# Optimization experiments

Measured on AMD Instinct MI355X. Metric: run time of the kernel, lower is better.

The kernel has to match this reference:

```python
import jax, jax.numpy as jnp
from jax import lax
import numpy as np

EPS = 1e-3  # Keras BatchNormalization default epsilon

def cond_conv(x, experts, rw, rb):
    # x: [B,H,W,Cin]; experts: [E,kh,kw,Cin,Cout]
    pooled = jnp.mean(x, axis=(1, 2))                       # [B,Cin]
    route = jax.nn.sigmoid(pooled @ rw + rb)                # [B,E]
    kernels = jnp.einsum('be,ehwio->bhwio', route, experts) # per-example kernel
    def conv1(xi, ki):
        return lax.conv_general_dilated(
            xi[None], ki, window_strides=(1, 1), padding='SAME',
            dimension_numbers=('NHWC', 'HWIO', 'NHWC'))[0]
    return jax.vmap(conv1)(x, kernels)

def bn_inf(x, gamma, beta, mean, var):
    inv = gamma * lax.rsqrt(var + EPS)
    return x * inv + (beta - mean * inv)

def maxpool2(x):
    return lax.reduce_window(x, -jnp.inf, lax.max,
                             (1, 2, 2, 1), (1, 2, 2, 1), 'SAME')

def se_block(x, w1, w2):
    s = jnp.mean(x, axis=(1, 2))          # [B,C]
    s = jax.nn.relu(s @ w1)
    s = jax.nn.sigmoid(s @ w2)
    return x * s[:, None, None, :]

def setup_inputs() -> dict:
    key = jax.random.key(0)
    ks = jax.random.split(key, 12)
    d = {
        'x': jax.random.normal(ks[0], (64, 128, 128, 6), jnp.float32),
        'experts1': jax.random.normal(ks[1], (3, 3, 3, 6, 32), jnp.float32) * 0.1,
        'route1_w': jax.random.normal(ks[2], (6, 3), jnp.float32) * 0.1,
        'route1_b': jnp.zeros((3,), jnp.float32),
        'bn1_gamma': jnp.ones((32,), jnp.float32), 'bn1_beta': jnp.zeros((32,), jnp.float32),
        'bn1_mean': jnp.zeros((32,), jnp.float32), 'bn1_var': jnp.ones((32,), jnp.float32),
        'se1_w1': jax.random.normal(ks[3], (32, 2), jnp.float32) * 0.1,
        'se1_w2': jax.random.normal(ks[4], (2, 32), jnp.float32) * 0.1,
        'experts2': jax.random.normal(ks[5], (3, 3, 3, 32, 64), jnp.float32) * 0.05,
        'route2_w': jax.random.normal(ks[6], (32, 3), jnp.float32) * 0.1,
        'route2_b': jnp.zeros((3,), jnp.float32),
        'bn2_gamma': jnp.ones((64,), jnp.float32), 'bn2_beta': jnp.zeros((64,), jnp.float32),
        'bn2_mean': jnp.zeros((64,), jnp.float32), 'bn2_var': jnp.ones((64,), jnp.float32),
        'se2_w1': jax.random.normal(ks[7], (64, 4), jnp.float32) * 0.1,
        'se2_w2': jax.random.normal(ks[8], (4, 64), jnp.float32) * 0.1,
        'experts3': jax.random.normal(ks[9], (3, 3, 3, 64, 128), jnp.float32) * 0.05,
        'route3_w': jax.random.normal(ks[10], (64, 3), jnp.float32) * 0.1,
        'route3_b': jnp.zeros((3,), jnp.float32),
        'bn3_gamma': jnp.ones((128,), jnp.float32), 'bn3_beta': jnp.zeros((128,), jnp.float32),
        'bn3_mean': jnp.zeros((128,), jnp.float32), 'bn3_var': jnp.ones((128,), jnp.float32),
    }
    return d

def reference(x, experts1, route1_w, route1_b, bn1_gamma, bn1_beta, bn1_mean, bn1_var,
              se1_w1, se1_w2, experts2, route2_w, route2_b, bn2_gamma, bn2_beta,
              bn2_mean, bn2_var, se2_w1, se2_w2, experts3, route3_w, route3_b,
              bn3_gamma, bn3_beta, bn3_mean, bn3_var):
    h = cond_conv(x, experts1, route1_w, route1_b)
    h = jax.nn.relu(bn_inf(h, bn1_gamma, bn1_beta, bn1_mean, bn1_var))
    h = maxpool2(h)                       # [B,64,64,32]
    h = se_block(h, se1_w1, se1_w2)
    h = cond_conv(h, experts2, route2_w, route2_b)
    h = jax.nn.relu(bn_inf(h, bn2_gamma, bn2_beta, bn2_mean, bn2_var))
    h = maxpool2(h)                       # [B,32,32,64]
    h = se_block(h, se2_w1, se2_w2)
    h = cond_conv(h, experts3, route3_w, route3_b)
    h = bn_inf(h, bn3_gamma, bn3_beta, bn3_mean, bn3_var)
    return jnp.mean(h, axis=(1, 2))       # [B,128]
```

## Files before the change

### kernel.cpp

```cpp
#include <hip/hip_runtime.h>

#define EPSBN 1e-3f

typedef unsigned short ushort_t;
typedef __attribute__((ext_vector_type(8))) short bf8;
typedef __attribute__((ext_vector_type(4))) float f4;

__device__ __forceinline__ float sigmoidf_(float z) {
  return 1.0f / (1.0f + expf(-z));
}

__device__ __forceinline__ ushort_t f2bf(float x) {
  union { float f; unsigned u; } v; v.f = x;
  unsigned r = (v.u + 0x7fffu + ((v.u >> 16) & 1u)) >> 16;
  return (ushort_t)r;
}

__global__ void k_mean_x(const float* __restrict__ x, float* __restrict__ part) {
  const int b = blockIdx.x >> 2;
  const int q = blockIdx.x & 3;
  const int tid = threadIdx.x;
  float acc[6] = {0.f, 0.f, 0.f, 0.f, 0.f, 0.f};
  const float* xb = x + (size_t)b * 98304 + (size_t)q * 24576;
  for (int p = 0; p < 4; ++p) {
    const float* base = xb + (size_t)p * 6144 + (size_t)tid * 24;
#pragma unroll
    for (int k = 0; k < 6; ++k) {
      const float4 v = *(const float4*)(base + k * 4);
      acc[(4 * k + 0) % 6] += v.x;
      acc[(4 * k + 1) % 6] += v.y;
      acc[(4 * k + 2) % 6] += v.z;
      acc[(4 * k + 3) % 6] += v.w;
    }
  }
#pragma unroll
  for (int c = 0; c < 6; ++c)
    for (int off = 32; off > 0; off >>= 1) acc[c] += __shfl_down(acc[c], off, 64);
  __shared__ float red[4][6];
  const int lane = tid & 63, w = tid >> 6;
  if (lane == 0) {
#pragma unroll
    for (int c = 0; c < 6; ++c) red[w][c] = acc[c];
  }
  __syncthreads();
  if (tid < 6) {
    part[blockIdx.x * 6 + tid] = red[0][tid] + red[1][tid] + red[2][tid] + red[3][tid];
  }
}

__global__ __launch_bounds__(256)
void k_conv1(const float* __restrict__ x, const float* __restrict__ meanx_part,
             const float* __restrict__ experts1,
             const float* __restrict__ rw, const float* __restrict__ rbias,
             const float* __restrict__ gamma, const float* __restrict__ beta,
             const float* __restrict__ bnmean, const float* __restrict__ bnvar,
             ushort_t* __restrict__ p1b, float* __restrict__ part_m1) {
  const int bid = blockIdx.x;
  const int b = bid >> 3;
  const int tyi = (bid >> 1) & 3;
  const int txi = bid & 1;
  __shared__ __align__(16) ushort_t patch[34 * 68 * 8];
  __shared__ float route_s[3];
  __shared__ float mred[4][32];
  const int tid = threadIdx.x;
  const float* xb = x + (size_t)b * (128 * 128 * 6);

  if (tid < 3) {
    float z = rbias[tid];
    for (int c = 0; c < 6; ++c) {
      const float s = meanx_part[(b * 4 + 0) * 6 + c] + meanx_part[(b * 4 + 1) * 6 + c] +
                      meanx_part[(b * 4 + 2) * 6 + c] + meanx_part[(b * 4 + 3) * 6 + c];
      z += (s * (1.0f / 16384.0f)) * rw[c * 3 + tid];
    }
    route_s[tid] = sigmoidf_(z);
  }

  for (int v = tid; v < 34 * 68; v += 256) {
    const int ry = v / 68, p = v - ry * 68;
    const int gy = tyi * 32 - 1 + ry, gx = txi * 64 - 1 + p;
    uint4 u = make_uint4(0u, 0u, 0u, 0u);
    if (((unsigned)gy < 128u) && ((unsigned)gx < 128u)) {
      const float* s = xb + ((size_t)(gy * 128 + gx)) * 6;
      const float2 a0 = *(const float2*)s;
      const float2 a1 = *(const float2*)(s + 2);
      const float2 a2 = *(const float2*)(s + 4);
      u.x = (unsigned)f2bf(a0.x) | ((unsigned)f2bf(a0.y) << 16);
      u.y = (unsigned)f2bf(a1.x) | ((unsigned)f2bf(a1.y) << 16);
      u.z = (unsigned)f2bf(a2.x) | ((unsigned)f2bf(a2.y) << 16);
      u.w = 0u;
    }
    *(uint4*)(patch + (size_t)v * 8) = u;
  }
  __syncthreads();

  const int w = tid >> 6;
  const int lane = tid & 63;
  const int lx = lane & 15, lg = lane >> 4;

  const float r0 = route_s[0], r1 = route_s[1], r2 = route_s[2];
  const int co0 = lx, co1 = 16 + lx;
  const float inv0 = gamma[co0] * rsqrtf(bnvar[co0] + EPSBN);
  const float bias0 = beta[co0] - bnmean[co0] * inv0;
  const float inv1 = gamma[co1] * rsqrtf(bnvar[co1] + EPSBN);
  const float bias1 = beta[co1] - bnmean[co1] * inv1;

  bf8 Bf[3][2];
#pragma unroll
  for (int ky = 0; ky < 3; ++ky) {
#pragma unroll
    for (int nt = 0; nt < 2; ++nt) {
      const int co = nt * 16 + lx;
      const float inv = nt ? inv1 : inv0;
#pragma unroll
      for (int j = 0; j < 8; ++j) {
        float val = 0.f;
        if (j < 6 && lg < 3) {
          const int idx = ((ky * 3 + lg) * 6 + j) * 32 + co;
          val = (r0 * experts1[idx] + r1 * experts1[1728 + idx] +
                 r2 * experts1[3456 + idx]) * inv;
        }
        Bf[ky][nt][j] = (short)f2bf(val);
      }
    }
  }

  float msum0 = 0.f, msum1 = 0.f;

#pragma unroll
  for (int xt = 0; xt < 4; ++xt) {
    bf8 Af[10];
#pragma unroll
    for (int r = 0; r < 10; ++r)
      Af[r] = *(const bf8*)(patch + ((size_t)(w * 8 + r) * 68 + xt * 16 + lx + lg) * 8);
#pragma unroll
    for (int rp = 0; rp < 4; ++rp) {
      const int prow = tyi * 16 + w * 4 + rp;
      f4 acc0[2], acc1[2];
#pragma unroll
      for (int nt = 0; nt < 2; ++nt) {
        acc0[nt] = (f4){0.f, 0.f, 0.f, 0.f};
        acc1[nt] = (f4){0.f, 0.f, 0.f, 0.f};
      }
#pragma unroll
      for (int ky = 0; ky < 3; ++ky) {
#pragma unroll
        for (int nt = 0; nt < 2; ++nt) {
          acc0[nt] = __builtin_amdgcn_mfma_f32_16x16x32_bf16(Af[rp * 2 + ky], Bf[ky][nt], acc0[nt], 0, 0, 0);
          acc1[nt] = __builtin_amdgcn_mfma_f32_16x16x32_bf16(Af[rp * 2 + ky + 1], Bf[ky][nt], acc1[nt], 0, 0, 0);
        }
      }
#pragma unroll
      for (int nt = 0; nt < 2; ++nt) {
        const float bias = nt ? bias1 : bias0;
        const int co = nt * 16 + lx;
#pragma unroll
        for (int q = 0; q < 2; ++q) {
          const float m0 = fmaxf(acc0[nt][2 * q] + bias, 0.f);
          const float m1 = fmaxf(acc0[nt][2 * q + 1] + bias, 0.f);
          const float m2 = fmaxf(acc1[nt][2 * q] + bias, 0.f);
          const float m3 = fmaxf(acc1[nt][2 * q + 1] + bias, 0.f);
          const float mx = fmaxf(fmaxf(m0, m1), fmaxf(m2, m3));
          if (nt) msum1 += mx; else msum0 += mx;
          const int pcol = txi * 32 + xt * 8 + lg * 2 + q;
          p1b[(((size_t)b * 64 + prow) * 64 + pcol) * 32 + co] = f2bf(mx);
        }
      }
    }
  }

  msum0 += __shfl_xor(msum0, 16, 64);
  msum0 += __shfl_xor(msum0, 32, 64);
  msum1 += __shfl_xor(msum1, 16, 64);
  msum1 += __shfl_xor(msum1, 32, 64);
  if (lg == 0) {
    mred[w][lx] = msum0;
    mred[w][16 + lx] = msum1;
  }
  __syncthreads();
  if (tid < 32) {
    part_m1[(size_t)bid * 32 + tid] =
        mred[0][tid] + mred[1][tid] + mred[2][tid] + mred[3][tid];
  }
}

__global__ void k_buildk2(const float* __restrict__ part_m1,
                          const float* __restrict__ experts2,
                          const float* __restrict__ rw, const float* __restrict__ rb,
                          const float* __restrict__ w1, const float* __restrict__ w2,
                          const float* __restrict__ gamma, const float* __restrict__ var,
                          ushort_t* __restrict__ k2pb) {
  const int b = blockIdx.x / 3;
  const int seg = blockIdx.x - b * 3;
  const int tid = threadIdx.x;
  __shared__ float m1[32], h[2], s1[32], route[3];
  if (tid < 32) {
    float s = 0.f;
#pragma unroll
    for (int k = 0; k < 8; ++k) s += part_m1[(size_t)(b * 8 + k) * 32 + tid];
    m1[tid] = s * (1.0f / 4096.0f);
  }
  __syncthreads();
  if (tid < 2) {
    float z = 0.f;
    for (int c = 0; c < 32; ++c) z += m1[c] * w1[c * 2 + tid];
    h[tid] = fmaxf(z, 0.f);
  }
  __syncthreads();
  if (tid < 32) s1[tid] = sigmoidf_(h[0] * w2[tid] + h[1] * w2[32 + tid]);
  __syncthreads();
  if (tid < 3) {
    float z = rb[tid];
    for (int c = 0; c < 32; ++c) z += m1[c] * s1[c] * rw[c * 3 + tid];
    route[tid] = sigmoidf_(z);
  }
  __syncthreads();
  const float r0 = route[0], r1 = route[1], r2 = route[2];
  const int t_lo = seg * 6144, t_hi = t_lo + 6144;
  for (int t = t_lo + tid; t < t_hi; t += 256) {
    const int co = t & 63;
    const int ci = (t >> 6) & 31;
    const int tap = t >> 11;
    const float inv = gamma[co] * rsqrtf(var[co] + EPSBN);
    const float v = r0 * experts2[t] + r1 * experts2[18432 + t] + r2 * experts2[2 * 18432 + t];
    k2pb[(size_t)b * 18432 + ((size_t)tap * 64 + co) * 32 + ci] = f2bf(v * s1[ci] * inv);
  }
}

__global__ __launch_bounds__(256)
void k_conv2(const ushort_t* __restrict__ p1b, const ushort_t* __restrict__ k2pb,
             const float* __restrict__ gamma, const float* __restrict__ beta,
             const float* __restrict__ bnmean, const float* __restrict__ bnvar,
             float* __restrict__ part_s3) {
  const int bi = blockIdx.x;
  const int b = bi >> 5;
  const int tile = (bi >> 1) & 15;
  const int cog = bi & 1;
  const int ty = tile >> 2, tx = tile & 3;
  __shared__ __align__(16) short smem[24480];
  short* As = smem;
  short* Bs = smem + 12960;
  const int tid = threadIdx.x;

  const ushort_t* pb = p1b + (size_t)b * 131072;
  for (int v = tid; v < 1296; v += 256) {
    const int cell = v >> 2, part = v & 3;
    const int ly = cell / 18, lx2 = cell - ly * 18;
    const int gy = ty * 16 - 1 + ly, gx = tx * 16 - 1 + lx2;
    uint4 d = make_uint4(0u, 0u, 0u, 0u);
    if (((unsigned)gy < 64u) && ((unsigned)gx < 64u))
      d = *(const uint4*)(pb + (((size_t)gy << 6) + gx) * 32 + part * 8);
    *(uint4*)(As + (ly * 18 + lx2) * 40 + part * 8) = d;
  }
  for (int v = tid; v < 1152; v += 256) {
    const int r = v >> 2, part = v & 3;
    const int t = r >> 5, n = r & 31;
    const uint4 d = *(const uint4*)(k2pb + (size_t)b * 18432 +
                                    ((size_t)(t * 64 + cog * 32 + n)) * 32 + part * 8);
    *(uint4*)(Bs + r * 40 + part * 8) = d;
  }
  __syncthreads();

  const int w = tid >> 6;
  const int lane = tid & 63;
  const int lx = lane & 15, lg = lane >> 4;

  f4 acc[4][2];
#pragma unroll
  for (int mt = 0; mt < 4; ++mt)
#pragma unroll
    for (int nt = 0; nt < 2; ++nt)
      acc[mt][nt] = (f4){0.f, 0.f, 0.f, 0.f};

#pragma unroll
  for (int kx = 0; kx < 3; ++kx) {
    bf8 Af[6];
#pragma unroll
    for (int r = 0; r < 6; ++r)
      Af[r] = *(const bf8*)(As + ((4 * w + r) * 18 + lx + kx) * 40 + (lg << 3));
#pragma unroll
    for (int ky = 0; ky < 3; ++ky) {
      const int t = ky * 3 + kx;
      const bf8 Bf0 = *(const bf8*)(Bs + ((t << 5) + lx) * 40 + (lg << 3));
      const bf8 Bf1 = *(const bf8*)(Bs + ((t << 5) + 16 + lx) * 40 + (lg << 3));
#pragma unroll
      for (int mt = 0; mt < 4; ++mt) {
        acc[mt][0] = __builtin_amdgcn_mfma_f32_16x16x32_bf16(Af[ky + mt], Bf0, acc[mt][0], 0, 0, 0);
        acc[mt][1] = __builtin_amdgcn_mfma_f32_16x16x32_bf16(Af[ky + mt], Bf1, acc[mt][1], 0, 0, 0);
      }
    }
  }

  float inv[2], bias[2];
#pragma unroll
  for (int nt = 0; nt < 2; ++nt) {
    const int co = cog * 32 + nt * 16 + lx;
    inv[nt] = gamma[co] * rsqrtf(bnvar[co] + EPSBN);
    bias[nt] = beta[co] - bnmean[co] * inv[nt];
  }
  float agg[2][9];
#pragma unroll
  for (int nt = 0; nt < 2; ++nt)
#pragma unroll
    for (int a = 0; a < 9; ++a) agg[nt][a] = 0.f;

#pragma unroll
  for (int half = 0; half < 2; ++half) {
    const int prow = ty * 8 + 2 * w + half;
    const bool rT = (prow == 0), rB = (prow == 31);
#pragma unroll
    for (int q = 0; q < 2; ++q) {
      const int pcol = tx * 8 + 2 * lg + q;
      const bool cL = (pcol == 0), cR = (pcol == 31);
#pragma unroll
      for (int nt = 0; nt < 2; ++nt) {
        const float m0 = fmaxf(acc[2 * half][nt][2 * q] + bias[nt], 0.f);
        const float m1 = fmaxf(acc[2 * half][nt][2 * q + 1] + bias[nt], 0.f);
        const float m2 = fmaxf(acc[2 * half + 1][nt][2 * q] + bias[nt], 0.f);
        const float m3 = fmaxf(acc[2 * half + 1][nt][2 * q + 1] + bias[nt], 0.f);
        const float mx = fmaxf(fmaxf(m0, m1), fmaxf(m2, m3));
        agg[nt][0] += mx;
        if (rT) agg[nt][1] += mx;
        if (rB) agg[nt][2] += mx;
        if (cL) agg[nt][3] += mx;
        if (cR) agg[nt][4] += mx;
        if (rT && cL) agg[nt][5] += mx;
        if (rT && cR) agg[nt][6] += mx;
        if (rB && cL) agg[nt][7] += mx;
        if (rB && cR) agg[nt][8] += mx;
      }
    }
  }

#pragma unroll
  for (int nt = 0; nt < 2; ++nt)
#pragma unroll
    for (int a = 0; a < 9; ++a) {
      float v = agg[nt][a];
      v += __shfl_xor(v, 16, 64);
      v += __shfl_xor(v, 32, 64);
      agg[nt][a] = v;
    }
  __syncthreads();
  float* sred = (float*)smem;
  if (lg == 0) {
#pragma unroll
    for (int nt = 0; nt < 2; ++nt)
#pragma unroll
      for (int a = 0; a < 9; ++a)
        sred[((w * 2 + nt) * 16 + lx) * 9 + a] = agg[nt][a];
  }
  __syncthreads();
  for (int v = tid; v < 288; v += 256) {
    const int a = v >> 5;
    const int colocal = v & 31;
    const int nt = colocal >> 4, lxx = colocal & 15;
    float s = 0.f;
#pragma unroll
    for (int ww = 0; ww < 4; ++ww) s += sred[((ww * 2 + nt) * 16 + lxx) * 9 + a];
    part_s3[(size_t)bi * 288 + v] = s;
  }
}

__global__ __launch_bounds__(512)
void k_final(const float* __restrict__ part_s3, const float* __restrict__ experts3,
             const float* __restrict__ rw, const float* __restrict__ rb,
             const float* __restrict__ w1, const float* __restrict__ w2,
             const float* __restrict__ gamma, const float* __restrict__ beta,
             const float* __restrict__ bnmean, const float* __restrict__ bnvar,
             float* __restrict__ out) {
  const int b = blockIdx.x;
  const int tid = threadIdx.x;
  __shared__ float AG[9][64], Sp[9][64], m2[64], h[4], s2[64], route[3], redf[4][128];

  for (int v = tid; v < 576; v += 512) {
    const int a = v >> 6, ci = v & 63;
    const int cg = ci >> 5, colocal = ci & 31;
    float s = 0.f;
#pragma unroll
    for (int tile = 0; tile < 16; ++tile)
      s += part_s3[(size_t)((b * 16 + tile) * 2 + cg) * 288 + a * 32 + colocal];
    AG[a][ci] = s;
  }
  __syncthreads();
  if (tid < 64) m2[tid] = AG[0][tid] * (1.0f / 1024.0f);
  __syncthreads();
  if (tid < 4) {
    float z = 0.f;
    for (int c = 0; c < 64; ++c) z += m2[c] * w1[c * 4 + tid];
    h[tid] = fmaxf(z, 0.f);
  }
  __syncthreads();
  if (tid < 64) {
    float z = 0.f;
#pragma unroll
    for (int j = 0; j < 4; ++j) z += h[j] * w2[j * 64 + tid];
    s2[tid] = sigmoidf_(z);
  }
  __syncthreads();
  if (tid < 3) {
    float z = rb[tid];
    for (int c = 0; c < 64; ++c) z += m2[c] * s2[c] * rw[c * 3 + tid];
    route[tid] = sigmoidf_(z);
  }
  __syncthreads();
  for (int v = tid; v < 576; v += 512) {
    const int tap = v >> 6, ci = v & 63;
    const int ky = tap / 3, kx = tap - 3 * ky;
    const float T = AG[0][ci];
    const float A = (ky == 0) ? AG[2][ci] : ((ky == 2) ? AG[1][ci] : 0.f);
    const float B = (kx == 0) ? AG[4][ci] : ((kx == 2) ? AG[3][ci] : 0.f);
    float AB = 0.f;
    if (ky == 0 && kx == 0) AB = AG[8][ci];
    else if (ky == 0 && kx == 2) AB = AG[7][ci];
    else if (ky == 2 && kx == 0) AB = AG[6][ci];
    else if (ky == 2 && kx == 2) AB = AG[5][ci];
    Sp[tap][ci] = (T - A - B + AB) * s2[ci];
  }
  __syncthreads();

  const int co = tid & 127;
  const int quarter = tid >> 7;
  const int tap_lo = (quarter == 0) ? 0 : (2 * quarter + 1);
  const int tap_hi = tap_lo + ((quarter == 0) ? 3 : 2);
  float acc = 0.f;
#pragma unroll
  for (int e = 0; e < 3; ++e) {
    float m = 0.f;
    for (int tap = tap_lo; tap < tap_hi; ++tap) {
      const float* E = experts3 + ((size_t)(e * 9 + tap) * 64) * 128 + co;
#pragma unroll 16
      for (int ci = 0; ci < 64; ++ci) m = fmaf(E[(size_t)ci * 128], Sp[tap][ci], m);
    }
    acc += route[e] * m;
  }
  redf[quarter][co] = acc;
  __syncthreads();
  if (tid < 128) {
    const float total = redf[0][tid] + redf[1][tid] + redf[2][tid] + redf[3][tid];
    const float inv = gamma[tid] * rsqrtf(bnvar[tid] + EPSBN);
    out[(size_t)b * 128 + tid] = total * (1.0f / 1024.0f) * inv + (beta[tid] - bnmean[tid] * inv);
  }
}

extern "C" void kernel_launch(void* const* d_in, const int* in_sizes, int n_in,
                              void* d_out, int out_size, void* d_ws, size_t ws_size,
                              hipStream_t stream) {
  const float* x        = (const float*)d_in[0];
  const float* experts1 = (const float*)d_in[1];
  const float* rw1      = (const float*)d_in[2];
  const float* rb1      = (const float*)d_in[3];
  const float* g1  = (const float*)d_in[4];
  const float* be1 = (const float*)d_in[5];
  const float* mu1 = (const float*)d_in[6];
  const float* va1 = (const float*)d_in[7];
  const float* sw1a = (const float*)d_in[8];
  const float* sw1b = (const float*)d_in[9];
  const float* experts2 = (const float*)d_in[10];
  const float* rw2 = (const float*)d_in[11];
  const float* rb2 = (const float*)d_in[12];
  const float* g2  = (const float*)d_in[13];
  const float* be2 = (const float*)d_in[14];
  const float* mu2 = (const float*)d_in[15];
  const float* va2 = (const float*)d_in[16];
  const float* sw2a = (const float*)d_in[17];
  const float* sw2b = (const float*)d_in[18];
  const float* experts3 = (const float*)d_in[19];
  const float* rw3 = (const float*)d_in[20];
  const float* rb3 = (const float*)d_in[21];
  const float* g3  = (const float*)d_in[22];
  const float* be3 = (const float*)d_in[23];
  const float* mu3 = (const float*)d_in[24];
  const float* va3 = (const float*)d_in[25];
  float* out = (float*)d_out;
  float* ws = (float*)d_ws;

  float* meanx_part = ws;
  float* part_m1    = ws + 1536;
  ushort_t* k2pb    = (ushort_t*)(ws + 17920);
  float* part_s3    = ws + 607744;
  ushort_t* p1b     = (ushort_t*)(ws + 1197568);

  hipLaunchKernelGGL(k_mean_x, dim3(256), dim3(256), 0, stream, x, meanx_part);
  hipLaunchKernelGGL(k_conv1, dim3(512), dim3(256), 0, stream,
                     x, meanx_part, experts1, rw1, rb1, g1, be1, mu1, va1, p1b, part_m1);
  hipLaunchKernelGGL(k_buildk2, dim3(192), dim3(256), 0, stream,
                     part_m1, experts2, rw2, rb2, sw1a, sw1b, g2, va2, k2pb);
  hipLaunchKernelGGL(k_conv2, dim3(2048), dim3(256), 0, stream,
                     p1b, k2pb, g2, be2, mu2, va2, part_s3);
  hipLaunchKernelGGL(k_final, dim3(64), dim3(512), 0, stream,
                     part_s3, experts3, rw3, rb3, sw2a, sw2b, g3, be3, mu3, va3, out);
}
```

Before: 187.9 us.

## Fuse all stages into one cooperative kernel with per-batch spin barriers

```diff
diff --git a/kernel.cpp b/kernel.cpp
--- a/kernel.cpp
+++ b/kernel.cpp
@@ -16,429 +16,442 @@
   return (ushort_t)r;
 }
 
-__global__ void k_mean_x(const float* __restrict__ x, float* __restrict__ part) {
-  const int b = blockIdx.x >> 2;
-  const int q = blockIdx.x & 3;
+__device__ __forceinline__ void batch_barrier(unsigned* ctr, unsigned target) {
+  __syncthreads();
+  if (threadIdx.x == 0) {
+    __threadfence();
+    atomicAdd(ctr, 1u);
+    while (atomicAdd(ctr, 0u) < target) __builtin_amdgcn_s_sleep(2);
+    __threadfence();
+  }
+  __syncthreads();
+}
+
+__global__ __launch_bounds__(256, 2)
+void k_fused(const float* __restrict__ x,
+             const float* __restrict__ experts1,
+             const float* __restrict__ rw1, const float* __restrict__ rb1,
+             const float* __restrict__ g1, const float* __restrict__ be1,
+             const float* __restrict__ mu1, const float* __restrict__ va1,
+             const float* __restrict__ sw1a, const float* __restrict__ sw1b,
+             const float* __restrict__ experts2,
+             const float* __restrict__ rw2, const float* __restrict__ rb2,
+             const float* __restrict__ g2, const float* __restrict__ be2,
+             const float* __restrict__ mu2, const float* __restrict__ va2,
+             const float* __restrict__ sw2a, const float* __restrict__ sw2b,
+             const float* __restrict__ experts3,
+             const float* __restrict__ rw3, const float* __restrict__ rb3,
+             const float* __restrict__ g3, const float* __restrict__ be3,
+             const float* __restrict__ mu3, const float* __restrict__ va3,
+             float* __restrict__ out,
+             float* __restrict__ meanx_part, float* __restrict__ part_m1,
+             ushort_t* __restrict__ k2pb, float* __restrict__ part_s3,
+             ushort_t* __restrict__ p1b, unsigned* __restrict__ bctr) {
+  __shared__ __align__(16) unsigned char smem[53568];
+  const int bid = blockIdx.x;
+  const int b = bid >> 3;
+  const int sub = bid & 7;
   const int tid = threadIdx.x;
-  float acc[6] = {0.f, 0.f, 0.f, 0.f, 0.f, 0.f};
-  const float* xb = x + (size_t)b * 98304 + (size_t)q * 24576;
-  for (int p = 0; p < 4; ++p) {
-    const float* base = xb + (size_t)p * 6144 + (size_t)tid * 24;
-#pragma unroll
-    for (int k = 0; k < 6; ++k) {
+  unsigned* ctr = bctr + b;
+
+  {
+    float acc[6] = {0.f, 0.f, 0.f, 0.f, 0.f, 0.f};
+    const float* base = x + (size_t)b * 98304 + (size_t)sub * 12288 + (size_t)tid * 48;
+#pragma unroll
+    for (int k = 0; k < 12; ++k) {
       const float4 v = *(const float4*)(base + k * 4);
       acc[(4 * k + 0) % 6] += v.x;
       acc[(4 * k + 1) % 6] += v.y;
       acc[(4 * k + 2) % 6] += v.z;
       acc[(4 * k + 3) % 6] += v.w;
     }
+#pragma unroll
+    for (int c = 0; c < 6; ++c)
+      for (int off = 32; off > 0; off >>= 1) acc[c] += __shfl_down(acc[c], off, 64);
+    float* red0 = (float*)smem;
+    const int lane = tid & 63, w = tid >> 6;
+    if (lane == 0) {
+#pragma unroll
+      for (int c = 0; c < 6; ++c) red0[w * 6 + c] = acc[c];
+    }
+    __syncthreads();
+    if (tid < 6)
+      meanx_part[bid * 6 + tid] = red0[tid] + red0[6 + tid] + red0[12 + tid] + red0[18 + tid];
   }
-#pragma unroll
-  for (int c = 0; c < 6; ++c)
-    for (int off = 32; off > 0; off >>= 1) acc[c] += __shfl_down(acc[c], off, 64);
-  __shared__ float red[4][6];
-  const int lane = tid & 63, w = tid >> 6;
-  if (lane == 0) {
-#pragma unroll
-    for (int c = 0; c < 6; ++c) red[w][c] = acc[c];
+  batch_barrier(ctr, 8u);
+
+  {
+    ushort_t* patch = (ushort_t*)smem;
+    float* route_s = (float*)(smem + 36992);
+    float* mred = (float*)(smem + 37008);
+    const int tyi = sub >> 1, txi = sub & 1;
+    const float* xb = x + (size_t)b * 98304;
+
+    if (tid < 3) {
+      float z = rb1[tid];
+      for (int c = 0; c < 6; ++c) {
+        float s = 0.f;
+#pragma unroll
+        for (int k = 0; k < 8; ++k) s += meanx_part[(b * 8 + k) * 6 + c];
+        z += (s * (1.0f / 16384.0f)) * rw1[c * 3 + tid];
+      }
+      route_s[tid] = sigmoidf_(z);
+    }
+
+    for (int v = tid; v < 34 * 68; v += 256) {
+      const int ry = v / 68, p = v - ry * 68;
+      const int gy = tyi * 32 - 1 + ry, gx = txi * 64 - 1 + p;
+      uint4 u = make_uint4(0u, 0u, 0u, 0u);
+      if (((unsigned)gy < 128u) && ((unsigned)gx < 128u)) {
+        const float* s = xb + ((size_t)(gy * 128 + gx)) * 6;
+        const float2 a0 = *(const float2*)s;
+        const float2 a1 = *(const float2*)(s + 2);
+        const float2 a2 = *(const float2*)(s + 4);
+        u.x = (unsigned)f2bf(a0.x) | ((unsigned)f2bf(a0.y) << 16);
+        u.y = (unsigned)f2bf(a1.x) | ((unsigned)f2bf(a1.y) << 16);
+        u.z = (unsigned)f2bf(a2.x) | ((unsigned)f2bf(a2.y) << 16);
+        u.w = 0u;
+      }
+      *(uint4*)(patch + (size_t)v * 8) = u;
+    }
+    __syncthreads();
+
+    const int w = tid >> 6;
+    const int lane = tid & 63;
+    const int lx = lane & 15, lg = lane >> 4;
+
+    const float r0 = route_s[0], r1 = route_s[1], r2 = route_s[2];
+    const int co0 = lx, co1 = 16 + lx;
+    const float inv0 = g1[co0] * rsqrtf(va1[co0] + EPSBN);
+    const float bias0 = be1[co0] - mu1[co0] * inv0;
+    const float inv1 = g1[co1] * rsqrtf(va1[co1] + EPSBN);
+    const float bias1 = be1[co1] - mu1[co1] * inv1;
+
+    bf8 Bf[3][2];
+#pragma unroll
+    for (int ky = 0; ky < 3; ++ky) {
+#pragma unroll
+      for (int nt = 0; nt < 2; ++nt) {
+        const int co = nt * 16 + lx;
+        const float inv = nt ? inv1 : inv0;
+#pragma unroll
+        for (int j = 0; j < 8; ++j) {
+          float val = 0.f;
+          if (j < 6 && lg < 3) {
+            const int idx = ((ky * 3 + lg) * 6 + j) * 32 + co;
+            val = (r0 * experts1[idx] + r1 * experts1[1728 + idx] +
+                   r2 * experts1[3456 + idx]) * inv;
+          }
+          Bf[ky][nt][j] = (short)f2bf(val);
+        }
+      }
+    }
+
+    float msum0 = 0.f, msum1 = 0.f;
+#pragma unroll
+    for (int xt = 0; xt < 4; ++xt) {
+      bf8 Af[10];
+#pragma unroll
+      for (int r = 0; r < 10; ++r)
+        Af[r] = *(const bf8*)(patch + ((size_t)(w * 8 + r) * 68 + xt * 16 + lx + lg) * 8);
+#pragma unroll
+      for (int rp = 0; rp < 4; ++rp) {
+        const int prow = tyi * 16 + w * 4 + rp;
+        f4 acc0[2], acc1[2];
+#pragma unroll
+        for (int nt = 0; nt < 2; ++nt) {
+          acc0[nt] = (f4){0.f, 0.f, 0.f, 0.f};
+          acc1[nt] = (f4){0.f, 0.f, 0.f, 0.f};
+        }
+#pragma unroll
+        for (int ky = 0; ky < 3; ++ky) {
+#pragma unroll
+          for (int nt = 0; nt < 2; ++nt) {
+            acc0[nt] = __builtin_amdgcn_mfma_f32_16x16x32_bf16(Af[rp * 2 + ky], Bf[ky][nt], acc0[nt], 0, 0, 0);
+            acc1[nt] = __builtin_amdgcn_mfma_f32_16x16x32_bf16(Af[rp * 2 + ky + 1], Bf[ky][nt], acc1[nt], 0, 0, 0);
+          }
+        }
+#pragma unroll
+        for (int nt = 0; nt < 2; ++nt) {
+          const float bias = nt ? bias1 : bias0;
+          const int co = nt * 16 + lx;
+#pragma unroll
+          for (int q = 0; q < 2; ++q) {
+            const float m0 = fmaxf(acc0[nt][2 * q] + bias, 0.f);
+            const float m1 = fmaxf(acc0[nt][2 * q + 1] + bias, 0.f);
+            const float m2 = fmaxf(acc1[nt][2 * q] + bias, 0.f);
+            const float m3 = fmaxf(acc1[nt][2 * q + 1] + bias, 0.f);
+            const float mx = fmaxf(fmaxf(m0, m1), fmaxf(m2, m3));
+            if (nt) msum1 += mx; else msum0 += mx;
+            const int pcol = txi * 32 + xt * 8 + lg * 2 + q;
+            p1b[(((size_t)b * 64 + prow) * 64 + pcol) * 32 + co] = f2bf(mx);
+          }
+        }
+      }
+    }
+
+    msum0 += __shfl_xor(msum0, 16, 64);
+    msum0 += __shfl_xor(msum0, 32, 64);
+    msum1 += __shfl_xor(msum1, 16, 64);
+    msum1 += __shfl_xor(msum1, 32, 64);
+    if (lg == 0) {
+      mred[w * 32 + lx] = msum0;
+      mred[w * 32 + 16 + lx] = msum1;
+    }
+    __syncthreads();
+    if (tid < 32) {
+      part_m1[(size_t)bid * 32 + tid] =
+          mred[tid] + mred[32 + tid] + mred[64 + tid] + mred[96 + tid];
+    }
   }
-  __syncthreads();
-  if (tid < 6) {
-    part[blockIdx.x * 6 + tid] = red[0][tid] + red[1][tid] + red[2][tid] + red[3][tid];
+  batch_barrier(ctr, 16u);
+
+  {
+    float* m1 = (float*)smem;
+    float* h = m1 + 32;
+    float* s1 = h + 4;
+    float* route = s1 + 32;
+    if (tid < 32) {
+      float s = 0.f;
+#pragma unroll
+      for (int k = 0; k < 8; ++k) s += part_m1[(size_t)(b * 8 + k) * 32 + tid];
+      m1[tid] = s * (1.0f / 4096.0f);
+    }
+    __syncthreads();
+    if (tid < 2) {
+      float z = 0.f;
+      for (int c = 0; c < 32; ++c) z += m1[c] * sw1a[c * 2 + tid];
+      h[tid] = fmaxf(z, 0.f);
+    }
+    __syncthreads();
+    if (tid < 32) s1[tid] = sigmoidf_(h[0] * sw1b[tid] + h[1] * sw1b[32 + tid]);
+    __syncthreads();
+    if (tid < 3) {
+      float z = rb2[tid];
+      for (int c = 0; c < 32; ++c) z += m1[c] * s1[c] * rw2[c * 3 + tid];
+      route[tid] = sigmoidf_(z);
+    }
+    __syncthreads();
+    const float r0 = route[0], r1 = route[1], r2 = route[2];
+    const int t_lo = sub * 2304, t_hi = t_lo + 2304;
+    for (int t = t_lo + tid; t < t_hi; t += 256) {
+      const int co = t & 63;
+      const int ci = (t >> 6) & 31;
+      const int tap = t >> 11;
+      const float inv = g2[co] * rsqrtf(va2[co] + EPSBN);
+      const float v = r0 * experts2[t] + r1 * experts2[18432 + t] + r2 * experts2[2 * 18432 + t];
+      k2pb[(size_t)b * 18432 + ((size_t)tap * 64 + co) * 32 + ci] = f2bf(v * s1[ci] * inv);
+    }
   }
-}
-
-__global__ __launch_bounds__(256)
-void k_conv1(const float* __restrict__ x, const float* __restrict__ meanx_part,
-             const float* __restrict__ experts1,
-             const float* __restrict__ rw, const float* __restrict__ rbias,
-             const float* __restrict__ gamma, const float* __restrict__ beta,
-             const float* __restrict__ bnmean, const float* __restrict__ bnvar,
-             ushort_t* __restrict__ p1b, float* __restrict__ part_m1) {
-  const int bid = blockIdx.x;
-  const int b = bid >> 3;
-  const int tyi = (bid >> 1) & 3;
-  const int txi = bid & 1;
-  __shared__ __align__(16) ushort_t patch[34 * 68 * 8];
-  __shared__ float route_s[3];
-  __shared__ float mred[4][32];
-  const int tid = threadIdx.x;
-  const float* xb = x + (size_t)b * (128 * 128 * 6);
-
-  if (tid < 3) {
-    float z = rbias[tid];
-    for (int c = 0; c < 6; ++c) {
-      const float s = meanx_part[(b * 4 + 0) * 6 + c] + meanx_part[(b * 4 + 1) * 6 + c] +
-                      meanx_part[(b * 4 + 2) * 6 + c] + meanx_part[(b * 4 + 3) * 6 + c];
-      z += (s * (1.0f / 16384.0f)) * rw[c * 3 + tid];
-    }
-    route_s[tid] = sigmoidf_(z);
+  batch_barrier(ctr, 24u);
+
+  {
+    short* As = (short*)smem;
+    short* Bs = As + 12960;
+    float* sred = (float*)(smem + 48960);
+    const int w = tid >> 6;
+    const int lane = tid & 63;
+    const int lx = lane & 15, lg = lane >> 4;
+    const ushort_t* pb = p1b + (size_t)b * 131072;
+
+    for (int cc = 0; cc < 4; ++cc) {
+      const int ti = sub * 4 + cc;
+      const int tile = ti >> 1, cog = ti & 1;
+      const int ty = tile >> 2, tx2 = tile & 3;
+      __syncthreads();
+      for (int v = tid; v < 1296; v += 256) {
+        const int cell = v >> 2, part = v & 3;
+        const int ly = cell / 18, lx2 = cell - ly * 18;
+        const int gy = ty * 16 - 1 + ly, gx = tx2 * 16 - 1 + lx2;
+        uint4 d = make_uint4(0u, 0u, 0u, 0u);
+        if (((unsigned)gy < 64u) && ((unsigned)gx < 64u))
+          d = *(const uint4*)(pb + (((size_t)gy << 6) + gx) * 32 + part * 8);
+        *(uint4*)(As + (ly * 18 + lx2) * 40 + part * 8) = d;
+      }
+      for (int v = tid; v < 1152; v += 256) {
+        const int r = v >> 2, part = v & 3;
+        const int t = r >> 5, n = r & 31;
+        const uint4 d = *(const uint4*)(k2pb + (size_t)b * 18432 +
+                                        ((size_t)(t * 64 + cog * 32 + n)) * 32 + part * 8);
+        *(uint4*)(Bs + r * 40 + part * 8) = d;
+      }
+      __syncthreads();
+
+      f4 acc[4][2];
+#pragma unroll
+      for (int mt = 0; mt < 4; ++mt)
+#pragma unroll
+        for (int nt = 0; nt < 2; ++nt)
+          acc[mt][nt] = (f4){0.f, 0.f, 0.f, 0.f};
+
+#pragma unroll
+      for (int kx = 0; kx < 3; ++kx) {
+        bf8 Af[6];
+#pragma unroll
+        for (int r = 0; r < 6; ++r)
+          Af[r] = *(const bf8*)(As + ((4 * w + r) * 18 + lx + kx) * 40 + (lg << 3));
+#pragma unroll
+        for (int ky = 0; ky < 3; ++ky) {
+          const int t = ky * 3 + kx;
+          const bf8 Bf0 = *(const bf8*)(Bs + ((t << 5) + lx) * 40 + (lg << 3));
+          const bf8 Bf1 = *(const bf8*)(Bs + ((t << 5) + 16 + lx) * 40 + (lg << 3));
+#pragma unroll
+          for (int mt = 0; mt < 4; ++mt) {
+            acc[mt][0] = __builtin_amdgcn_mfma_f32_16x16x32_bf16(Af[ky + mt], Bf0, acc[mt][0], 0, 0, 0);
+            acc[mt][1] = __builtin_amdgcn_mfma_f32_16x16x32_bf16(Af[ky + mt], Bf1, acc[mt][1], 0, 0, 0);
+          }
+        }
+      }
+
+      float inv[2], bias[2];
+#pragma unroll
+      for (int nt = 0; nt < 2; ++nt) {
+        const int co = cog * 32 + nt * 16 + lx;
+        inv[nt] = g2[co] * rsqrtf(va2[co] + EPSBN);
+        bias[nt] = be2[co] - mu2[co] * inv[nt];
+      }
+      float agg[2][9];
+#pragma unroll
+      for (int nt = 0; nt < 2; ++nt)
+#pragma unroll
+        for (int a = 0; a < 9; ++a) agg[nt][a] = 0.f;
+
+#pragma unroll
+      for (int half = 0; half < 2; ++half) {
+        const int prow = ty * 8 + 2 * w + half;
+        const bool rT = (prow == 0), rB = (prow == 31);
+#pragma unroll
+        for (int q = 0; q < 2; ++q) {
+          const int pcol = tx2 * 8 + 2 * lg + q;
+          const bool cL = (pcol == 0), cR = (pcol == 31);
+#pragma unroll
+          for (int nt = 0; nt < 2; ++nt) {
+            const float m0 = fmaxf(acc[2 * half][nt][2 * q] + bias[nt], 0.f);
+            const float m1 = fmaxf(acc[2 * half][nt][2 * q + 1] + bias[nt], 0.f);
+            const float m2 = fmaxf(acc[2 * half + 1][nt][2 * q] + bias[nt], 0.f);
+            const float m3 = fmaxf(acc[2 * half + 1][nt][2 * q + 1] + bias[nt], 0.f);
+            const float mx = fmaxf(fmaxf(m0, m1), fmaxf(m2, m3));
+            agg[nt][0] += mx;
+            if (rT) agg[nt][1] += mx;
+            if (rB) agg[nt][2] += mx;
+            if (cL) agg[nt][3] += mx;
+            if (cR) agg[nt][4] += mx;
+            if (rT && cL) agg[nt][5] += mx;
+            if (rT && cR) agg[nt][6] += mx;
+            if (rB && cL) agg[nt][7] += mx;
+            if (rB && cR) agg[nt][8] += mx;
+          }
+        }
+      }
+
+#pragma unroll
+      for (int nt = 0; nt < 2; ++nt)
+#pragma unroll
+        for (int a = 0; a < 9; ++a) {
+          float v = agg[nt][a];
+          v += __shfl_xor(v, 16, 64);
+          v += __shfl_xor(v, 32, 64);
+          agg[nt][a] = v;
+        }
+      if (lg == 0) {
+#pragma unroll
+        for (int nt = 0; nt < 2; ++nt)
+#pragma unroll
+          for (int a = 0; a < 9; ++a)
+            sred[((w * 2 + nt) * 16 + lx) * 9 + a] = agg[nt][a];
+      }
+      __syncthreads();
+      for (int v = tid; v < 288; v += 256) {
+        const int a = v >> 5;
+        const int colocal = v & 31;
+        const int nt = colocal >> 4, lxx = colocal & 15;
+        float s = 0.f;
+#pragma unroll
+        for (int ww = 0; ww < 4; ++ww) s += sred[((ww * 2 + nt) * 16 + lxx) * 9 + a];
+        part_s3[(size_t)(b * 32 + ti) * 288 + v] = s;
+      }
+    }
   }
-
-  for (int v = tid; v < 34 * 68; v += 256) {
-    const int ry = v / 68, p = v - ry * 68;
-    const int gy = tyi * 32 - 1 + ry, gx = txi * 64 - 1 + p;
-    uint4 u = make_uint4(0u, 0u, 0u, 0u);
-    if (((unsigned)gy < 128u) && ((unsigned)gx < 128u)) {
-      const float* s = xb + ((size_t)(gy * 128 + gx)) * 6;
-      const float2 a0 = *(const float2*)s;
-      const float2 a1 = *(const float2*)(s + 2);
-      const float2 a2 = *(const float2*)(s + 4);
-      u.x = (unsigned)f2bf(a0.x) | ((unsigned)f2bf(a0.y) << 16);
-      u.y = (unsigned)f2bf(a1.x) | ((unsigned)f2bf(a1.y) << 16);
-      u.z = (unsigned)f2bf(a2.x) | ((unsigned)f2bf(a2.y) << 16);
-      u.w = 0u;
-    }
-    *(uint4*)(patch + (size_t)v * 8) = u;
-  }
-  __syncthreads();
-
-  const int w = tid >> 6;
-  const int lane = tid & 63;
-  const int lx = lane & 15, lg = lane >> 4;
-
-  const float r0 = route_s[0], r1 = route_s[1], r2 = route_s[2];
-  const int co0 = lx, co1 = 16 + lx;
-  const float inv0 = gamma[co0] * rsqrtf(bnvar[co0] + EPSBN);
-  const float bias0 = beta[co0] - bnmean[co0] * inv0;
-  const float inv1 = gamma[co1] * rsqrtf(bnvar[co1] + EPSBN);
-  const float bias1 = beta[co1] - bnmean[co1] * inv1;
-
-  bf8 Bf[3][2];
-#pragma unroll
-  for (int ky = 0; ky < 3; ++ky) {
-#pragma unroll
-    for (int nt = 0; nt < 2; ++nt) {
-      const int co = nt * 16 + lx;
-      const float inv = nt ? inv1 : inv0;
-#pragma unroll
-      for (int j = 0; j < 8; ++j) {
-        float val = 0.f;
-        if (j < 6 && lg < 3) {
-          const int idx = ((ky * 3 + lg) * 6 + j) * 32 + co;
-          val = (r0 * experts1[idx] + r1 * experts1[1728 + idx] +
-                 r2 * experts1[3456 + idx]) * inv;
-        }
-        Bf[ky][nt][j] = (short)f2bf(val);
-      }
-    }
-  }
-
-  float msum0 = 0.f, msum1 = 0.f;
-
-#pragma unroll
-  for (int xt = 0; xt < 4; ++xt) {
-    bf8 Af[10];
-#pragma unroll
-    for (int r = 0; r < 10; ++r)
-      Af[r] = *(const bf8*)(patch + ((size_t)(w * 8 + r) * 68 + xt * 16 + lx + lg) * 8);
-#pragma unroll
-    for (int rp = 0; rp < 4; ++rp) {
-      const int prow = tyi * 16 + w * 4 + rp;
-      f4 acc0[2], acc1[2];
-#pragma unroll
-      for (int nt = 0; nt < 2; ++nt) {
-        acc0[nt] = (f4){0.f, 0.f, 0.f, 0.f};
-        acc1[nt] = (f4){0.f, 0.f, 0.f, 0.f};
-      }
-#pragma unroll
-      for (int ky = 0; ky < 3; ++ky) {
-#pragma unroll
-        for (int nt = 0; nt < 2; ++nt) {
-          acc0[nt] = __builtin_amdgcn_mfma_f32_16x16x32_bf16(Af[rp * 2 + ky], Bf[ky][nt], acc0[nt], 0, 0, 0);
-          acc1[nt] = __builtin_amdgcn_mfma_f32_16x16x32_bf16(Af[rp * 2 + ky + 1], Bf[ky][nt], acc1[nt], 0, 0, 0);
-        }
-      }
-#pragma unroll
-      for (int nt = 0; nt < 2; ++nt) {
-        const float bias = nt ? bias1 : bias0;
-        const int co = nt * 16 + lx;
-#pragma unroll
-        for (int q = 0; q < 2; ++q) {
-          const float m0 = fmaxf(acc0[nt][2 * q] + bias, 0.f);
-          const float m1 = fmaxf(acc0[nt][2 * q + 1] + bias, 0.f);
-          const float m2 = fmaxf(acc1[nt][2 * q] + bias, 0.f);
-          const float m3 = fmaxf(acc1[nt][2 * q + 1] + bias, 0.f);
-          const float mx = fmaxf(fmaxf(m0, m1), fmaxf(m2, m3));
-          if (nt) msum1 += mx; else msum0 += mx;
-          const int pcol = txi * 32 + xt * 8 + lg * 2 + q;
-          p1b[(((size_t)b * 64 + prow) * 64 + pcol) * 32 + co] = f2bf(mx);
-        }
-      }
-    }
-  }
-
-  msum0 += __shfl_xor(msum0, 16, 64);
-  msum0 += __shfl_xor(msum0, 32, 64);
-  msum1 += __shfl_xor(msum1, 16, 64);
-  msum1 += __shfl_xor(msum1, 32, 64);
-  if (lg == 0) {
-    mred[w][lx] = msum0;
-    mred[w][16 + lx] = msum1;
-  }
-  __syncthreads();
-  if (tid < 32) {
-    part_m1[(size_t)bid * 32 + tid] =
-        mred[0][tid] + mred[1][tid] + mred[2][tid] + mred[3][tid];
-  }
-}
-
-__global__ void k_buildk2(const float* __restrict__ part_m1,
-                          const float* __restrict__ experts2,
-                          const float* __restrict__ rw, const float* __restrict__ rb,
-                          const float* __restrict__ w1, const float* __restrict__ w2,
-                          const float* __restrict__ gamma, const float* __restrict__ var,
-                          ushort_t* __restrict__ k2pb) {
-  const int b = blockIdx.x / 3;
-  const int seg = blockIdx.x - b * 3;
-  const int tid = threadIdx.x;
-  __shared__ float m1[32], h[2], s1[32], route[3];
-  if (tid < 32) {
-    float s = 0.f;
-#pragma unroll
-    for (int k = 0; k < 8; ++k) s += part_m1[(size_t)(b * 8 + k) * 32 + tid];
-    m1[tid] = s * (1.0f / 4096.0f);
-  }
-  __syncthreads();
-  if (tid < 2) {
-    float z = 0.f;
-    for (int c = 0; c < 32; ++c) z += m1[c] * w1[c * 2 + tid];
-    h[tid] = fmaxf(z, 0.f);
-  }
-  __syncthreads();
-  if (tid < 32) s1[tid] = sigmoidf_(h[0] * w2[tid] + h[1] * w2[32 + tid]);
-  __syncthreads();
-  if (tid < 3) {
-    float z = rb[tid];
-    for (int c = 0; c < 32; ++c) z += m1[c] * s1[c] * rw[c * 3 + tid];
-    route[tid] = sigmoidf_(z);
-  }
-  __syncthreads();
-  const float r0 = route[0], r1 = route[1], r2 = route[2];
-  const int t_lo = seg * 6144, t_hi = t_lo + 6144;
-  for (int t = t_lo + tid; t < t_hi; t += 256) {
-    const int co = t & 63;
-    const int ci = (t >> 6) & 31;
-    const int tap = t >> 11;
-    const float inv = gamma[co] * rsqrtf(var[co] + EPSBN);
-    const float v = r0 * experts2[t] + r1 * experts2[18432 + t] + r2 * experts2[2 * 18432 + t];
-    k2pb[(size_t)b * 18432 + ((size_t)tap * 64 + co) * 32 + ci] = f2bf(v * s1[ci] * inv);
-  }
-}
-
-__global__ __launch_bounds__(256)
-void k_conv2(const ushort_t* __restrict__ p1b, const ushort_t* __restrict__ k2pb,
-             const float* __restrict__ gamma, const float* __restrict__ beta,
-             const float* __restrict__ bnmean, const float* __restrict__ bnvar,
-             float* __restrict__ part_s3) {
-  const int bi = blockIdx.x;
-  const int b = bi >> 5;
-  const int tile = (bi >> 1) & 15;
-  const int cog = bi & 1;
-  const int ty = tile >> 2, tx = tile & 3;
-  __shared__ __align__(16) short smem[24480];
-  short* As = smem;
-  short* Bs = smem + 12960;
-  const int tid = threadIdx.x;
-
-  const ushort_t* pb = p1b + (size_t)b * 131072;
-  for (int v = tid; v < 1296; v += 256) {
-    const int cell = v >> 2, part = v & 3;
-    const int ly = cell / 18, lx2 = cell - ly * 18;
-    const int gy = ty * 16 - 1 + ly, gx = tx * 16 - 1 + lx2;
-    uint4 d = make_uint4(0u, 0u, 0u, 0u);
-    if (((unsigned)gy < 64u) && ((unsigned)gx < 64u))
-      d = *(const uint4*)(pb + (((size_t)gy << 6) + gx) * 32 + part * 8);
-    *(uint4*)(As + (ly * 18 + lx2) * 40 + part * 8) = d;
-  }
-  for (int v = tid; v < 1152; v += 256) {
-    const int r = v >> 2, part = v & 3;
-    const int t = r >> 5, n = r & 31;
-    const uint4 d = *(const uint4*)(k2pb + (size_t)b * 18432 +
-                                    ((size_t)(t * 64 + cog * 32 + n)) * 32 + part * 8);
-    *(uint4*)(Bs + r * 40 + part * 8) = d;
-  }
-  __syncthreads();
-
-  const int w = tid >> 6;
-  const int lane = tid & 63;
-  const int lx = lane & 15, lg = lane >> 4;
-
-  f4 acc[4][2];
-#pragma unroll
-  for (int mt = 0; mt < 4; ++mt)
-#pragma unroll
-    for (int nt = 0; nt < 2; ++nt)
-      acc[mt][nt] = (f4){0.f, 0.f, 0.f, 0.f};
-
-#pragma unroll
-  for (int kx = 0; kx < 3; ++kx) {
-    bf8 Af[6];
-#pragma unroll
-    for (int r = 0; r < 6; ++r)
-      Af[r] = *(const bf8*)(As + ((4 * w + r) * 18 + lx + kx) * 40 + (lg << 3));
-#pragma unroll
-    for (int ky = 0; ky < 3; ++ky) {
-      const int t = ky * 3 + kx;
-      const bf8 Bf0 = *(const bf8*)(Bs + ((t << 5) + lx) * 40 + (lg << 3));
-      const bf8 Bf1 = *(const bf8*)(Bs + ((t << 5) + 16 + lx) * 40 + (lg << 3));
-#pragma unroll
-      for (int mt = 0; mt < 4; ++mt) {
-        acc[mt][0] = __builtin_amdgcn_mfma_f32_16x16x32_bf16(Af[ky + mt], Bf0, acc[mt][0], 0, 0, 0);
-        acc[mt][1] = __builtin_amdgcn_mfma_f32_16x16x32_bf16(Af[ky + mt], Bf1, acc[mt][1], 0, 0, 0);
-      }
-    }
-  }
-
-  float inv[2], bias[2];
-#pragma unroll
-  for (int nt = 0; nt < 2; ++nt) {
-    const int co = cog * 32 + nt * 16 + lx;
-    inv[nt] = gamma[co] * rsqrtf(bnvar[co] + EPSBN);
-    bias[nt] = beta[co] - bnmean[co] * inv[nt];
-  }
-  float agg[2][9];
-#pragma unroll
-  for (int nt = 0; nt < 2; ++nt)
-#pragma unroll
-    for (int a = 0; a < 9; ++a) agg[nt][a] = 0.f;
-
-#pragma unroll
-  for (int half = 0; half < 2; ++half) {
-    const int prow = ty * 8 + 2 * w + half;
-    const bool rT = (prow == 0), rB = (prow == 31);
-#pragma unroll
-    for (int q = 0; q < 2; ++q) {
-      const int pcol = tx * 8 + 2 * lg + q;
-      const bool cL = (pcol == 0), cR = (pcol == 31);
-#pragma unroll
-      for (int nt = 0; nt < 2; ++nt) {
-        const float m0 = fmaxf(acc[2 * half][nt][2 * q] + bias[nt], 0.f);
-        const float m1 = fmaxf(acc[2 * half][nt][2 * q + 1] + bias[nt], 0.f);
-        const float m2 = fmaxf(acc[2 * half + 1][nt][2 * q] + bias[nt], 0.f);
-        const float m3 = fmaxf(acc[2 * half + 1][nt][2 * q + 1] + bias[nt], 0.f);
-        const float mx = fmaxf(fmaxf(m0, m1), fmaxf(m2, m3));
-        agg[nt][0] += mx;
-        if (rT) agg[nt][1] += mx;
-        if (rB) agg[nt][2] += mx;
-        if (cL) agg[nt][3] += mx;
-        if (cR) agg[nt][4] += mx;
-        if (rT && cL) agg[nt][5] += mx;
-        if (rT && cR) agg[nt][6] += mx;
-        if (rB && cL) agg[nt][7] += mx;
-        if (rB && cR) agg[nt][8] += mx;
-      }
-    }
-  }
-
-#pragma unroll
-  for (int nt = 0; nt < 2; ++nt)
-#pragma unroll
-    for (int a = 0; a < 9; ++a) {
-      float v = agg[nt][a];
-      v += __shfl_xor(v, 16, 64);
-      v += __shfl_xor(v, 32, 64);
-      agg[nt][a] = v;
-    }
-  __syncthreads();
-  float* sred = (float*)smem;
-  if (lg == 0) {
-#pragma unroll
-    for (int nt = 0; nt < 2; ++nt)
-#pragma unroll
-      for (int a = 0; a < 9; ++a)
-        sred[((w * 2 + nt) * 16 + lx) * 9 + a] = agg[nt][a];
-  }
-  __syncthreads();
-  for (int v = tid; v < 288; v += 256) {
-    const int a = v >> 5;
-    const int colocal = v & 31;
-    const int nt = colocal >> 4, lxx = colocal & 15;
-    float s = 0.f;
-#pragma unroll
-    for (int ww = 0; ww < 4; ++ww) s += sred[((ww * 2 + nt) * 16 + lxx) * 9 + a];
-    part_s3[(size_t)bi * 288 + v] = s;
-  }
-}
-
-__global__ __launch_bounds__(512)
-void k_final(const float* __restrict__ part_s3, const float* __restrict__ experts3,
-             const float* __restrict__ rw, const float* __restrict__ rb,
-             const float* __restrict__ w1, const float* __restrict__ w2,
-             const float* __restrict__ gamma, const float* __restrict__ beta,
-             const float* __restrict__ bnmean, const float* __restrict__ bnvar,
-             float* __restrict__ out) {
-  const int b = blockIdx.x;
-  const int tid = threadIdx.x;
-  __shared__ float AG[9][64], Sp[9][64], m2[64], h[4], s2[64], route[3], redf[4][128];
-
-  for (int v = tid; v < 576; v += 512) {
-    const int a = v >> 6, ci = v & 63;
-    const int cg = ci >> 5, colocal = ci & 31;
-    float s = 0.f;
-#pragma unroll
-    for (int tile = 0; tile < 16; ++tile)
-      s += part_s3[(size_t)((b * 16 + tile) * 2 + cg) * 288 + a * 32 + colocal];
-    AG[a][ci] = s;
-  }
-  __syncthreads();
-  if (tid < 64) m2[tid] = AG[0][tid] * (1.0f / 1024.0f);
-  __syncthreads();
-  if (tid < 4) {
-    float z = 0.f;
-    for (int c = 0; c < 64; ++c) z += m2[c] * w1[c * 4 + tid];
-    h[tid] = fmaxf(z, 0.f);
-  }
-  __syncthreads();
-  if (tid < 64) {
-    float z = 0.f;
-#pragma unroll
-    for (int j = 0; j < 4; ++j) z += h[j] * w2[j * 64 + tid];
-    s2[tid] = sigmoidf_(z);
-  }
-  __syncthreads();
-  if (tid < 3) {
-    float z = rb[tid];
-    for (int c = 0; c < 64; ++c) z += m2[c] * s2[c] * rw[c * 3 + tid];
-    route[tid] = sigmoidf_(z);
-  }
-  __syncthreads();
-  for (int v = tid; v < 576; v += 512) {
-    const int tap = v >> 6, ci = v & 63;
-    const int ky = tap / 3, kx = tap - 3 * ky;
-    const float T = AG[0][ci];
-    const float A = (ky == 0) ? AG[2][ci] : ((ky == 2) ? AG[1][ci] : 0.f);
-    const float B = (kx == 0) ? AG[4][ci] : ((kx == 2) ? AG[3][ci] : 0.f);
-    float AB = 0.f;
-    if (ky == 0 && kx == 0) AB = AG[8][ci];
-    else if (ky == 0 && kx == 2) AB = AG[7][ci];
-    else if (ky == 2 && kx == 0) AB = AG[6][ci];
-    else if (ky == 2 && kx == 2) AB = AG[5][ci];
-    Sp[tap][ci] = (T - A - B + AB) * s2[ci];
-  }
-  __syncthreads();
-
-  const int co = tid & 127;
-  const int quarter = tid >> 7;
-  const int tap_lo = (quarter == 0) ? 0 : (2 * quarter + 1);
-  const int tap_hi = tap_lo + ((quarter == 0) ? 3 : 2);
-  float acc = 0.f;
-#pragma unroll
-  for (int e = 0; e < 3; ++e) {
-    float m = 0.f;
-    for (int tap = tap_lo; tap < tap_hi; ++tap) {
-      const float* E = experts3 + ((size_t)(e * 9 + tap) * 64) * 128 + co;
+  batch_barrier(ctr, 32u);
+
+  if (sub != 0) return;
+  {
+    float* AG = (float*)smem;
+    float* Sp = AG + 576;
+    float* m2 = Sp + 576;
+    float* h = m2 + 64;
+    float* s2 = h + 4;
+    float* route = s2 + 64;
+    float* redf = route + 4;
+
+    for (int v = tid; v < 576; v += 256) {
+      const int a = v >> 6, ci = v & 63;
+      const int cg = ci >> 5, colocal = ci & 31;
+      float s = 0.f;
+#pragma unroll
+      for (int tile = 0; tile < 16; ++tile)
+        s += part_s3[(size_t)(b * 32 + 2 * tile + cg) * 288 + a * 32 + colocal];
+      AG[a * 64 + ci] = s;
+    }
+    __syncthreads();
+    if (tid < 64) m2[tid] = AG[tid] * (1.0f / 1024.0f);
+    __syncthreads();
+    if (tid < 4) {
+      float z = 0.f;
+      for (int c = 0; c < 64; ++c) z += m2[c] * sw2a[c * 4 + tid];
+      h[tid] = fmaxf(z, 0.f);
+    }
+    __syncthreads();
+    if (tid < 64) {
+      float z = 0.f;
+#pragma unroll
+      for (int j = 0; j < 4; ++j) z += h[j] * sw2b[j * 64 + tid];
+      s2[tid] = sigmoidf_(z);
+    }
+    __syncthreads();
+    if (tid < 3) {
+      float z = rb3[tid];
+      for (int c = 0; c < 64; ++c) z += m2[c] * s2[c] * rw3[c * 3 + tid];
+      route[tid] = sigmoidf_(z);
+    }
+    __syncthreads();
+    for (int v = tid; v < 576; v += 256) {
+      const int tap = v >> 6, ci = v & 63;
+      const int ky = tap / 3, kx = tap - 3 * ky;
+      const float T = AG[ci];
+      const float A = (ky == 0) ? AG[2 * 64 + ci] : ((ky == 2) ? AG[1 * 64 + ci] : 0.f);
+      const float B = (kx == 0) ? AG[4 * 64 + ci] : ((kx == 2) ? AG[3 * 64 + ci] : 0.f);
+      float AB = 0.f;
+      if (ky == 0 && kx == 0) AB = AG[8 * 64 + ci];
+      else if (ky == 0 && kx == 2) AB = AG[7 * 64 + ci];
+      else if (ky == 2 && kx == 0) AB = AG[6 * 64 + ci];
+      else if (ky == 2 && kx == 2) AB = AG[5 * 64 + ci];
+      Sp[tap * 64 + ci] = (T - A - B + AB) * s2[ci];
+    }
+    __syncthreads();
+
+    const int co = tid & 127;
+    const int half = tid >> 7;
+    const int tap_lo = half ? 5 : 0;
+    const int tap_hi = half ? 9 : 5;
+    float acc = 0.f;
+#pragma unroll
+    for (int e = 0; e < 3; ++e) {
+      float m = 0.f;
+      for (int tap = tap_lo; tap < tap_hi; ++tap) {
+        const float* E = experts3 + ((size_t)(e * 9 + tap) * 64) * 128 + co;
 #pragma unroll 16
-      for (int ci = 0; ci < 64; ++ci) m = fmaf(E[(size_t)ci * 128], Sp[tap][ci], m);
-    }
-    acc += route[e] * m;
-  }
-  redf[quarter][co] = acc;
-  __syncthreads();
-  if (tid < 128) {
-    const float total = redf[0][tid] + redf[1][tid] + redf[2][tid] + redf[3][tid];
-    const float inv = gamma[tid] * rsqrtf(bnvar[tid] + EPSBN);
-    out[(size_t)b * 128 + tid] = total * (1.0f / 1024.0f) * inv + (beta[tid] - bnmean[tid] * inv);
+        for (int ci = 0; ci < 64; ++ci) m = fmaf(E[(size_t)ci * 128], Sp[tap * 64 + ci], m);
+      }
+      acc += route[e] * m;
+    }
+    redf[half * 128 + co] = acc;
+    __syncthreads();
+    if (tid < 128) {
+      const float total = redf[tid] + redf[128 + tid];
+      const float inv = g3[tid] * rsqrtf(va3[tid] + EPSBN);
+      out[(size_t)b * 128 + tid] = total * (1.0f / 1024.0f) * inv + (be3[tid] - mu3[tid] * inv);
+    }
   }
 }
 
@@ -475,18 +488,24 @@
   float* ws = (float*)d_ws;
 
   float* meanx_part = ws;
-  float* part_m1    = ws + 1536;
-  ushort_t* k2pb    = (ushort_t*)(ws + 17920);
-  float* part_s3    = ws + 607744;
-  ushort_t* p1b     = (ushort_t*)(ws + 1197568);
-
-  hipLaunchKernelGGL(k_mean_x, dim3(256), dim3(256), 0, stream, x, meanx_part);
-  hipLaunchKernelGGL(k_conv1, dim3(512), dim3(256), 0, stream,
-                     x, meanx_part, experts1, rw1, rb1, g1, be1, mu1, va1, p1b, part_m1);
-  hipLaunchKernelGGL(k_buildk2, dim3(192), dim3(256), 0, stream,
-                     part_m1, experts2, rw2, rb2, sw1a, sw1b, g2, va2, k2pb);
-  hipLaunchKernelGGL(k_conv2, dim3(2048), dim3(256), 0, stream,
-                     p1b, k2pb, g2, be2, mu2, va2, part_s3);
-  hipLaunchKernelGGL(k_final, dim3(64), dim3(512), 0, stream,
-                     part_s3, experts3, rw3, rb3, sw2a, sw2b, g3, be3, mu3, va3, out);
+  float* part_m1    = ws + 3072;
+  ushort_t* k2pb    = (ushort_t*)(ws + 19456);
+  float* part_s3    = ws + 609280;
+  ushort_t* p1b     = (ushort_t*)(ws + 1199104);
+  unsigned* bctr    = (unsigned*)(ws + 5393408);
+
+  hipMemsetAsync(bctr, 0, 64 * sizeof(unsigned), stream);
+
+  void* args[] = {
+    (void*)&x, (void*)&experts1, (void*)&rw1, (void*)&rb1,
+    (void*)&g1, (void*)&be1, (void*)&mu1, (void*)&va1,
+    (void*)&sw1a, (void*)&sw1b, (void*)&experts2,
+    (void*)&rw2, (void*)&rb2, (void*)&g2, (void*)&be2,
+    (void*)&mu2, (void*)&va2, (void*)&sw2a, (void*)&sw2b,
+    (void*)&experts3, (void*)&rw3, (void*)&rb3, (void*)&g3,
+    (void*)&be3, (void*)&mu3, (void*)&va3, (void*)&out,
+    (void*)&meanx_part, (void*)&part_m1, (void*)&k2pb,
+    (void*)&part_s3, (void*)&p1b, (void*)&bctr
+  };
+  hipLaunchCooperativeKernel((const void*)k_fused, dim3(512), dim3(256), args, 0, stream);
 }
```

Measured after the change: 409.0 us. 2.18x slower.
